# Kernel tuning notes

Measured on AMD Instinct MI355X. Metric: run time of the kernel, lower is better.

Reference implementation:

```python
import jax, jax.numpy as jnp
import numpy as np

B, L, HSIZE = 16, 512, 1024
H, D = 16, 64  # HHEAD = HSIZE/base, HBASE = 64

def setup_inputs() -> dict:
    key = jax.random.key(0)
    ks = jax.random.split(key, 10)
    inp = {
        'v': jax.random.normal(ks[0], (B, L, HSIZE), jnp.float32),
        'k': jax.random.normal(ks[1], (B, L, HSIZE), jnp.float32),
        'q': jax.random.normal(ks[2], (B, L, HSIZE), jnp.float32),
        'img_abs': jax.random.normal(ks[3], (B, L, HSIZE), jnp.float32),
        'Wv': jax.random.normal(ks[4], (HSIZE, HSIZE), jnp.float32) * 0.02,
        'Wk': jax.random.normal(ks[5], (HSIZE, HSIZE), jnp.float32) * 0.02,
        'Wq': jax.random.normal(ks[6], (HSIZE, HSIZE), jnp.float32) * 0.02,
        'Wm': jax.random.normal(ks[7], (HSIZE, HSIZE), jnp.float32) * 0.02,
        'abs_mask': jax.random.bernoulli(ks[8], 0.1, (B, 1, L, L)),
        'mask': jax.random.bernoulli(ks[9], 0.1, (B, 1, L, L)),
    }
    return inp

def reference(v, k, q, img_abs, Wv, Wk, Wq, Wm, abs_mask, mask):
    nb = q.shape[0]
    # Linear (no bias) then split heads: [B, L, HSIZE] -> [B, H, L, D]
    def heads(x):
        return x.reshape(nb, -1, H, D).transpose(0, 2, 1, 3)
    vh = heads(v @ Wv.T)
    kh = heads(k @ Wk.T)
    qh = heads(q @ Wq.T)
    ph = heads(img_abs)
    scale = 1.0 / jnp.sqrt(jnp.asarray(D, qh.dtype))
    # modulate: attention of q over positional features, residual-added to q
    s1 = jnp.einsum('bhqd,bhpd->bhqp', qh, ph) * scale
    s1 = jnp.where(abs_mask, jnp.asarray(-1e9, s1.dtype), s1)
    qh = qh + jnp.einsum('bhqp,bhpd->bhqd', jax.nn.softmax(s1, axis=-1), ph)
    # main attention (dropout = identity in eval mode)
    s2 = jnp.einsum('bhqd,bhkd->bhqk', qh, kh) * scale
    s2 = jnp.where(mask, jnp.asarray(-1e9, s2.dtype), s2)
    atted = jnp.einsum('bhqk,bhkd->bhqd', jax.nn.softmax(s2, axis=-1), vh)
    atted = atted.transpose(0, 2, 1, 3).reshape(nb, -1, H * D)
    return atted @ Wm.T
```

## Files before the change

kernel.cpp:

```cpp
#include <hip/hip_runtime.h>

typedef unsigned short u16;
typedef unsigned int u32;
typedef unsigned long long u64;
typedef __attribute__((ext_vector_type(8))) short short8;
typedef __attribute__((ext_vector_type(4))) float f32x4;

#define NB 16
#define SL 512
#define HS 1024
#define NHEAD 16
#define HD 64

typedef const __attribute__((address_space(1))) u32* gas_t;
typedef __attribute__((address_space(3))) u32* las_t;

__device__ __forceinline__ void gld16(const u16* g, u16* l) {
  __builtin_amdgcn_global_load_lds((gas_t)g, (las_t)l, 16, 0, 0);
}

__device__ __forceinline__ u16 f2bf(float f) {
  union { float f; unsigned u; } c; c.f = f;
  unsigned r = c.u + 0x7FFFu + ((c.u >> 16) & 1u);
  return (u16)(r >> 16);
}
__device__ __forceinline__ float bf2f(u16 u) {
  union { float f; unsigned u; } c; c.u = ((unsigned)u) << 16;
  return c.f;
}

__global__ __launch_bounds__(256) void cvt_bf16(const float* __restrict__ in,
                                                u16* __restrict__ out, long n) {
  long i = ((long)blockIdx.x * 256 + threadIdx.x) * 4;
  if (i >= n) return;
  float4 f = *(const float4*)(in + i);
  uint2 u;
  u.x = (unsigned)f2bf(f.x) | ((unsigned)f2bf(f.y) << 16);
  u.y = (unsigned)f2bf(f.z) | ((unsigned)f2bf(f.w) << 16);
  *(uint2*)(out + i) = u;
}

__global__ __launch_bounds__(256) void cvt_w4(const float* __restrict__ a,
                                              const float* __restrict__ b,
                                              const float* __restrict__ c,
                                              const float* __restrict__ d,
                                              u16* __restrict__ o, long n) {
  const float* in = (blockIdx.y == 0) ? a : (blockIdx.y == 1) ? b
                     : (blockIdx.y == 2) ? c : d;
  u16* out = o + (long)blockIdx.y * n;
  long i = ((long)blockIdx.x * 256 + threadIdx.x) * 4;
  if (i >= n) return;
  float4 f = *(const float4*)(in + i);
  uint2 u;
  u.x = (unsigned)f2bf(f.x) | ((unsigned)f2bf(f.y) << 16);
  u.y = (unsigned)f2bf(f.z) | ((unsigned)f2bf(f.w) << 16);
  *(uint2*)(out + i) = u;
}

__global__ __launch_bounds__(256) void pack_mask(const int* __restrict__ m0,
                                                 const int* __restrict__ m1,
                                                 u64* __restrict__ o0,
                                                 u64* __restrict__ o1, long n) {
  long i = (long)blockIdx.x * 256 + threadIdx.x;
  const int* m = blockIdx.y ? m1 : m0;
  u64* o = blockIdx.y ? o1 : o0;
  u64 bits = __ballot(m[i] != 0);
  if ((threadIdx.x & 63) == 0) o[i >> 6] = bits;
}

template<bool CF32>
__global__ __launch_bounds__(256) void gemm_bt(const u16* __restrict__ A,
                                               const u16* __restrict__ W,
                                               void* __restrict__ C,
                                               int M, int N, int K) {
  __shared__ u16 As[128 * 64];
  __shared__ u16 Bs[128 * 64];
  const int tid = threadIdx.x;
  const int wave = tid >> 6, lane = tid & 63;
  const int quad = lane >> 4, l16 = lane & 15;
  const int l7 = l16 & 7;
  const int row0 = blockIdx.x * 128, col0 = blockIdx.y * 128;
  const int wm = (wave >> 1) * 64, wn = (wave & 1) * 64;
  const int lrow = lane >> 3;
  const int scb = (lane & 7) ^ lrow;

  f32x4 acc[4][4];
#pragma unroll
  for (int mt = 0; mt < 4; ++mt)
#pragma unroll
    for (int nt = 0; nt < 4; ++nt) acc[mt][nt] = (f32x4){0.f, 0.f, 0.f, 0.f};

  const u16* Ab = A + (long)row0 * K;
  const u16* Wb = W + (long)col0 * K;

  for (int k0 = 0; k0 < K; k0 += 64) {
    __syncthreads();
#pragma unroll
    for (int it = 0; it < 4; ++it) {
      int seg = wave * 4 + it;
      int r = seg * 8 + lrow;
      gld16(Ab + (long)r * K + k0 + scb * 8, As + seg * 512);
      gld16(Wb + (long)r * K + k0 + scb * 8, Bs + seg * 512);
    }
    __syncthreads();
#pragma unroll
    for (int kt = 0; kt < 2; ++kt) {
      short8 af[4], bw[4];
#pragma unroll
      for (int mt = 0; mt < 4; ++mt)
        af[mt] = *(const short8*)(As + (wm + mt * 16 + l16) * 64 +
                                  (((kt * 4 + quad) ^ l7) * 8));
#pragma unroll
      for (int nt = 0; nt < 4; ++nt)
        bw[nt] = *(const short8*)(Bs + (wn + nt * 16 + l16) * 64 +
                                  (((kt * 4 + quad) ^ l7) * 8));
#pragma unroll
      for (int mt = 0; mt < 4; ++mt)
#pragma unroll
        for (int nt = 0; nt < 4; ++nt)
          acc[mt][nt] = __builtin_amdgcn_mfma_f32_16x16x32_bf16(
              af[mt], bw[nt], acc[mt][nt], 0, 0, 0);
    }
  }
#pragma unroll
  for (int mt = 0; mt < 4; ++mt)
#pragma unroll
    for (int nt = 0; nt < 4; ++nt)
#pragma unroll
      for (int i = 0; i < 4; ++i) {
        long r = row0 + wm + mt * 16 + quad * 4 + i;
        long c = col0 + wn + nt * 16 + l16;
        float v = acc[mt][nt][i];
        if constexpr (CF32)
          ((float*)C)[r * N + c] = v;
        else
          ((u16*)C)[r * N + c] = f2bf(v);
      }
}

__global__ __launch_bounds__(256) void attn(const u16* __restrict__ Qp,
                                            const u16* __restrict__ Kp,
                                            const u16* __restrict__ Vp,
                                            const u32* __restrict__ Bits,
                                            u16* __restrict__ Op,
                                            int residual) {
  __shared__ u16 Qs[64][72];
  __shared__ u16 Ks[64][72];
  __shared__ u16 Vs[64][72];
  __shared__ u16 Ps[64][72];
  const int tid = threadIdx.x;
  const int wave = tid >> 6, lane = tid & 63;
  const int quad = lane >> 4, l16 = lane & 15;
  const int qt = blockIdx.x, h = blockIdx.y, b = blockIdx.z;
  const int q0 = qt * 64;
  const long bs = (long)SL * HS;
  const u16* Qb = Qp + (long)b * bs + h * HD;
  const u16* Kb = Kp + (long)b * bs + h * HD;
  const u16* Vb = Vp + (long)b * bs + h * HD;
  const u32* Mb = Bits + (long)b * SL * 16;

  const int sr = tid >> 2, sds = (tid & 3) * 16;
  {
    const uint4* s = (const uint4*)(Qb + (long)(q0 + sr) * HS + sds);
    *(uint4*)&Qs[sr][sds] = s[0];
    *(uint4*)&Qs[sr][sds + 8] = s[1];
  }

  float l_i[4] = {0.f, 0.f, 0.f, 0.f};
  f32x4 o[4];
#pragma unroll
  for (int nt = 0; nt < 4; ++nt) o[nt] = (f32x4){0.f, 0.f, 0.f, 0.f};

  const int vxor = ((sds >> 4) & 3) << 4;
  const int vcol = sr ^ vxor;

  for (int t = 0; t < 8; ++t) {
    const int k0 = t * 64;
    __syncthreads();
    {
      const uint4* sk = (const uint4*)(Kb + (long)(k0 + sr) * HS + sds);
      *(uint4*)&Ks[sr][sds] = sk[0];
      *(uint4*)&Ks[sr][sds + 8] = sk[1];
      uint4 v0 = *(const uint4*)(Vb + (long)(k0 + sr) * HS + sds);
      uint4 v1 = *(const uint4*)(Vb + (long)(k0 + sr) * HS + sds + 8);
      union { uint4 q[2]; u16 e[16]; } tv;
      tv.q[0] = v0; tv.q[1] = v1;
#pragma unroll
      for (int j = 0; j < 16; ++j) Vs[sds + j][vcol] = tv.e[j];
    }
    __syncthreads();
    f32x4 s[4];
#pragma unroll
    for (int nt = 0; nt < 4; ++nt) s[nt] = (f32x4){0.f, 0.f, 0.f, 0.f};
#pragma unroll
    for (int kt = 0; kt < 2; ++kt) {
      short8 aq = *(const short8*)&Qs[wave * 16 + l16][kt * 32 + quad * 8];
#pragma unroll
      for (int nt = 0; nt < 4; ++nt) {
        short8 bk = *(const short8*)&Ks[nt * 16 + l16][kt * 32 + quad * 8];
        s[nt] = __builtin_amdgcn_mfma_f32_16x16x32_bf16(aq, bk, s[nt], 0, 0, 0);
      }
    }
#pragma unroll
    for (int i = 0; i < 4; ++i) {
      int gr = q0 + wave * 16 + quad * 4 + i;
      uint2 mw = *(const uint2*)&Mb[(long)gr * 16 + t * 2];
#pragma unroll
      for (int nt = 0; nt < 4; ++nt) {
        u32 w = (nt & 2) ? mw.y : mw.x;
        int msk = (w >> ((nt & 1) * 16 + l16)) & 1;
        float p = msk ? 0.f : __expf(s[nt][i] * 0.125f);
        s[nt][i] = p;
        l_i[i] += p;
      }
    }
#pragma unroll
    for (int i = 0; i < 4; ++i) {
      int prow = wave * 16 + quad * 4 + i;
#pragma unroll
      for (int nt = 0; nt < 4; ++nt)
        Ps[prow][(nt * 16 + l16) ^ (quad << 3)] = f2bf(s[nt][i]);
    }
    __syncthreads();
#pragma unroll
    for (int kt = 0; kt < 2; ++kt) {
      short8 ap = *(const short8*)&Ps[wave * 16 + l16]
                                    [(kt * 32 + quad * 8) ^ ((l16 >> 2) << 3)];
#pragma unroll
      for (int nt = 0; nt < 4; ++nt) {
        short8 bv = *(const short8*)&Vs[nt * 16 + l16]
                                      [(kt * 32 + quad * 8) ^ ((nt & 3) << 4)];
        o[nt] = __builtin_amdgcn_mfma_f32_16x16x32_bf16(ap, bv, o[nt], 0, 0, 0);
      }
    }
  }
  u16* Ob = Op + (long)b * bs + h * HD;
#pragma unroll
  for (int i = 0; i < 4; ++i) {
    float rs = l_i[i];
#pragma unroll
    for (int off = 8; off >= 1; off >>= 1) rs += __shfl_xor(rs, off, 64);
    float inv = 1.f / rs;
    int r = q0 + wave * 16 + quad * 4 + i;
#pragma unroll
    for (int nt = 0; nt < 4; ++nt) {
      float val = o[nt][i] * inv;
      if (residual) val += bf2f(Qs[wave * 16 + quad * 4 + i][nt * 16 + l16]);
      Ob[(long)r * HS + nt * 16 + l16] = f2bf(val);
    }
  }
}

extern "C" void kernel_launch(void* const* d_in, const int* in_sizes, int n_in,
                              void* d_out, int out_size, void* d_ws,
                              size_t ws_size, hipStream_t stream) {
  const float* v   = (const float*)d_in[0];
  const float* k   = (const float*)d_in[1];
  const float* q   = (const float*)d_in[2];
  const float* img = (const float*)d_in[3];
  const float* Wv  = (const float*)d_in[4];
  const float* Wk  = (const float*)d_in[5];
  const float* Wq  = (const float*)d_in[6];
  const float* Wm  = (const float*)d_in[7];
  const int* absm  = (const int*)d_in[8];
  const int* mask  = (const int*)d_in[9];
  float* out = (float*)d_out;

  const long NTOK = (long)NB * SL * HS;
  const long NW   = (long)HS * HS;
  const long NM   = (long)NB * SL * SL;
  u16* ws  = (u16*)d_ws;
  u16* xb  = ws;
  u16* pb  = ws + 1 * NTOK;
  u16* vh  = ws + 2 * NTOK;
  u16* kh  = ws + 3 * NTOK;
  u16* qh  = ws + 4 * NTOK;
  u16* w4  = ws + 5 * NTOK;
  u64* bt0 = (u64*)(w4 + 4 * NW);
  u64* bt1 = bt0 + NM / 64;
  u16* qm  = xb;
  u16* att = qh;

  dim3 gg(NB * SL / 128, HS / 128);
  dim3 ga(SL / 64, NHEAD, NB);

  cvt_bf16<<<(unsigned)(NTOK / 1024), 256, 0, stream>>>(img, pb, NTOK);
  cvt_w4<<<dim3((unsigned)(NW / 1024), 4), 256, 0, stream>>>(Wv, Wk, Wq, Wm, w4, NW);
  pack_mask<<<dim3((unsigned)(NM / 256), 2), 256, 0, stream>>>(absm, mask, bt0, bt1, NM);

  cvt_bf16<<<(unsigned)(NTOK / 1024), 256, 0, stream>>>(v, xb, NTOK);
  gemm_bt<false><<<gg, 256, 0, stream>>>(xb, w4 + 0 * NW, vh, NB * SL, HS, HS);
  cvt_bf16<<<(unsigned)(NTOK / 1024), 256, 0, stream>>>(k, xb, NTOK);
  gemm_bt<false><<<gg, 256, 0, stream>>>(xb, w4 + 1 * NW, kh, NB * SL, HS, HS);
  cvt_bf16<<<(unsigned)(NTOK / 1024), 256, 0, stream>>>(q, xb, NTOK);
  gemm_bt<false><<<gg, 256, 0, stream>>>(xb, w4 + 2 * NW, qh, NB * SL, HS, HS);

  attn<<<ga, 256, 0, stream>>>(qh, pb, pb, (const u32*)bt0, qm, 1);
  attn<<<ga, 256, 0, stream>>>(qm, kh, vh, (const u32*)bt1, att, 0);

  gemm_bt<true><<<gg, 256, 0, stream>>>(att, w4 + 3 * NW, out, NB * SL, HS, HS);
}
```

Before: 418.2 us.

## Batch input conversions and QKV projections, shrink output GEMM tile, register Q in attention

Fuses the four fp32-to-bf16 conversions into one launch, staging converted v and k in the output buffer as scratch. The three projection GEMMs become a single grouped launch selected by block index. The output projection gets a smaller 64x128 tile kernel with a higher occupancy hint, giving more blocks. In attention, Q fragments are loaded straight into registers instead of shared memory, the residual is read from global, and the XOR swizzle on the P tile is removed. The P-swizzle removal may bring back LDS bank conflicts.

```diff
diff --git a/kernel.cpp b/kernel.cpp
--- a/kernel.cpp
+++ b/kernel.cpp
@@ -11,6 +11,8 @@
 #define HS 1024
 #define NHEAD 16
 #define HD 64
+#define NTOKC (16L * 512 * 1024)
+#define NWC   (1024L * 1024)
 
 typedef const __attribute__((address_space(1))) u32* gas_t;
 typedef __attribute__((address_space(3))) u32* las_t;
@@ -29,8 +31,16 @@
   return c.f;
 }
 
-__global__ __launch_bounds__(256) void cvt_bf16(const float* __restrict__ in,
-                                                u16* __restrict__ out, long n) {
+__global__ __launch_bounds__(256) void cvt4(const float* __restrict__ v,
+                                            const float* __restrict__ k,
+                                            const float* __restrict__ q,
+                                            const float* __restrict__ img,
+                                            u16* __restrict__ ovk,
+                                            u16* __restrict__ xq,
+                                            u16* __restrict__ pb, long n) {
+  int which = blockIdx.y;
+  const float* in = which == 0 ? v : which == 1 ? k : which == 2 ? q : img;
+  u16* out = which == 0 ? ovk : which == 1 ? ovk + n : which == 2 ? xq : pb;
   long i = ((long)blockIdx.x * 256 + threadIdx.x) * 4;
   if (i >= n) return;
   float4 f = *(const float4*)(in + i);
@@ -68,21 +78,26 @@
   if ((threadIdx.x & 63) == 0) o[i >> 6] = bits;
 }
 
-template<bool CF32>
-__global__ __launch_bounds__(256) void gemm_bt(const u16* __restrict__ A,
-                                               const u16* __restrict__ W,
-                                               void* __restrict__ C,
-                                               int M, int N, int K) {
+__global__ __launch_bounds__(256) void gemm_p3(const u16* __restrict__ Avk,
+                                               const u16* __restrict__ Aq,
+                                               const u16* __restrict__ W4,
+                                               u16* __restrict__ Cb) {
   __shared__ u16 As[128 * 64];
   __shared__ u16 Bs[128 * 64];
   const int tid = threadIdx.x;
   const int wave = tid >> 6, lane = tid & 63;
   const int quad = lane >> 4, l16 = lane & 15;
   const int l7 = l16 & 7;
-  const int row0 = blockIdx.x * 128, col0 = blockIdx.y * 128;
+  const int sel = blockIdx.x >> 6;
+  const int row0 = (blockIdx.x & 63) * 128, col0 = blockIdx.y * 128;
   const int wm = (wave >> 1) * 64, wn = (wave & 1) * 64;
   const int lrow = lane >> 3;
   const int scb = (lane & 7) ^ lrow;
+  const int K = HS, N = HS;
+
+  const u16* A = (sel == 2) ? Aq : Avk + (long)sel * NTOKC;
+  const u16* W = W4 + (long)sel * NWC;
+  u16* C = Cb + (long)sel * NTOKC;
 
   f32x4 acc[4][4];
 #pragma unroll
@@ -130,11 +145,75 @@
       for (int i = 0; i < 4; ++i) {
         long r = row0 + wm + mt * 16 + quad * 4 + i;
         long c = col0 + wn + nt * 16 + l16;
-        float v = acc[mt][nt][i];
-        if constexpr (CF32)
-          ((float*)C)[r * N + c] = v;
-        else
-          ((u16*)C)[r * N + c] = f2bf(v);
+        C[r * N + c] = f2bf(acc[mt][nt][i]);
+      }
+}
+
+__global__ __launch_bounds__(256, 4) void gemm_f(const u16* __restrict__ A,
+                                                 const u16* __restrict__ W,
+                                                 float* __restrict__ C) {
+  __shared__ u16 As[64 * 64];
+  __shared__ u16 Bs[128 * 64];
+  const int tid = threadIdx.x;
+  const int wave = tid >> 6, lane = tid & 63;
+  const int quad = lane >> 4, l16 = lane & 15;
+  const int l7 = l16 & 7;
+  const int row0 = blockIdx.x * 64, col0 = blockIdx.y * 128;
+  const int wm = (wave >> 1) * 32, wn = (wave & 1) * 64;
+  const int lrow = lane >> 3;
+  const int scb = (lane & 7) ^ lrow;
+  const int K = HS, N = HS;
+
+  f32x4 acc[2][4];
+#pragma unroll
+  for (int mt = 0; mt < 2; ++mt)
+#pragma unroll
+    for (int nt = 0; nt < 4; ++nt) acc[mt][nt] = (f32x4){0.f, 0.f, 0.f, 0.f};
+
+  const u16* Ab = A + (long)row0 * K;
+  const u16* Wb = W + (long)col0 * K;
+
+  for (int k0 = 0; k0 < K; k0 += 64) {
+    __syncthreads();
+#pragma unroll
+    for (int it = 0; it < 2; ++it) {
+      int seg = wave * 2 + it;
+      gld16(Ab + (long)(seg * 8 + lrow) * K + k0 + scb * 8, As + seg * 512);
+    }
+#pragma unroll
+    for (int it = 0; it < 4; ++it) {
+      int seg = wave * 4 + it;
+      gld16(Wb + (long)(seg * 8 + lrow) * K + k0 + scb * 8, Bs + seg * 512);
+    }
+    __syncthreads();
+#pragma unroll
+    for (int kt = 0; kt < 2; ++kt) {
+      short8 af[2], bw[4];
+#pragma unroll
+      for (int mt = 0; mt < 2; ++mt)
+        af[mt] = *(const short8*)(As + (wm + mt * 16 + l16) * 64 +
+                                  (((kt * 4 + quad) ^ l7) * 8));
+#pragma unroll
+      for (int nt = 0; nt < 4; ++nt)
+        bw[nt] = *(const short8*)(Bs + (wn + nt * 16 + l16) * 64 +
+                                  (((kt * 4 + quad) ^ l7) * 8));
+#pragma unroll
+      for (int mt = 0; mt < 2; ++mt)
+#pragma unroll
+        for (int nt = 0; nt < 4; ++nt)
+          acc[mt][nt] = __builtin_amdgcn_mfma_f32_16x16x32_bf16(
+              af[mt], bw[nt], acc[mt][nt], 0, 0, 0);
+    }
+  }
+#pragma unroll
+  for (int mt = 0; mt < 2; ++mt)
+#pragma unroll
+    for (int nt = 0; nt < 4; ++nt)
+#pragma unroll
+      for (int i = 0; i < 4; ++i) {
+        long r = row0 + wm + mt * 16 + quad * 4 + i;
+        long c = col0 + wn + nt * 16 + l16;
+        C[r * N + c] = acc[mt][nt][i];
       }
 }
 
@@ -144,7 +223,6 @@
                                             const u32* __restrict__ Bits,
                                             u16* __restrict__ Op,
                                             int residual) {
-  __shared__ u16 Qs[64][72];
   __shared__ u16 Ks[64][72];
   __shared__ u16 Vs[64][72];
   __shared__ u16 Ps[64][72];
@@ -159,11 +237,11 @@
   const u16* Vb = Vp + (long)b * bs + h * HD;
   const u32* Mb = Bits + (long)b * SL * 16;
 
-  const int sr = tid >> 2, sds = (tid & 3) * 16;
-  {
-    const uint4* s = (const uint4*)(Qb + (long)(q0 + sr) * HS + sds);
-    *(uint4*)&Qs[sr][sds] = s[0];
-    *(uint4*)&Qs[sr][sds + 8] = s[1];
+  short8 qf[2];
+#pragma unroll
+  for (int kt = 0; kt < 2; ++kt) {
+    int row = q0 + wave * 16 + l16;
+    qf[kt] = *(const short8*)(Qb + (long)row * HS + kt * 32 + quad * 8);
   }
 
   float l_i[4] = {0.f, 0.f, 0.f, 0.f};
@@ -171,8 +249,8 @@
 #pragma unroll
   for (int nt = 0; nt < 4; ++nt) o[nt] = (f32x4){0.f, 0.f, 0.f, 0.f};
 
-  const int vxor = ((sds >> 4) & 3) << 4;
-  const int vcol = sr ^ vxor;
+  const int sr = tid >> 2, sds = (tid & 3) * 16;
+  const int vcol = sr ^ (((sds >> 4) & 3) << 4);
 
   for (int t = 0; t < 8; ++t) {
     const int k0 = t * 64;
@@ -193,14 +271,12 @@
 #pragma unroll
     for (int nt = 0; nt < 4; ++nt) s[nt] = (f32x4){0.f, 0.f, 0.f, 0.f};
 #pragma unroll
-    for (int kt = 0; kt < 2; ++kt) {
-      short8 aq = *(const short8*)&Qs[wave * 16 + l16][kt * 32 + quad * 8];
+    for (int kt = 0; kt < 2; ++kt)
 #pragma unroll
       for (int nt = 0; nt < 4; ++nt) {
         short8 bk = *(const short8*)&Ks[nt * 16 + l16][kt * 32 + quad * 8];
-        s[nt] = __builtin_amdgcn_mfma_f32_16x16x32_bf16(aq, bk, s[nt], 0, 0, 0);
-      }
-    }
+        s[nt] = __builtin_amdgcn_mfma_f32_16x16x32_bf16(qf[kt], bk, s[nt], 0, 0, 0);
+      }
 #pragma unroll
     for (int i = 0; i < 4; ++i) {
       int gr = q0 + wave * 16 + quad * 4 + i;
@@ -210,22 +286,14 @@
         u32 w = (nt & 2) ? mw.y : mw.x;
         int msk = (w >> ((nt & 1) * 16 + l16)) & 1;
         float p = msk ? 0.f : __expf(s[nt][i] * 0.125f);
-        s[nt][i] = p;
         l_i[i] += p;
-      }
-    }
-#pragma unroll
-    for (int i = 0; i < 4; ++i) {
-      int prow = wave * 16 + quad * 4 + i;
-#pragma unroll
-      for (int nt = 0; nt < 4; ++nt)
-        Ps[prow][(nt * 16 + l16) ^ (quad << 3)] = f2bf(s[nt][i]);
+        Ps[wave * 16 + quad * 4 + i][nt * 16 + l16] = f2bf(p);
+      }
     }
     __syncthreads();
 #pragma unroll
     for (int kt = 0; kt < 2; ++kt) {
-      short8 ap = *(const short8*)&Ps[wave * 16 + l16]
-                                    [(kt * 32 + quad * 8) ^ ((l16 >> 2) << 3)];
+      short8 ap = *(const short8*)&Ps[wave * 16 + l16][kt * 32 + quad * 8];
 #pragma unroll
       for (int nt = 0; nt < 4; ++nt) {
         short8 bv = *(const short8*)&Vs[nt * 16 + l16]
@@ -245,7 +313,7 @@
 #pragma unroll
     for (int nt = 0; nt < 4; ++nt) {
       float val = o[nt][i] * inv;
-      if (residual) val += bf2f(Qs[wave * 16 + quad * 4 + i][nt * 16 + l16]);
+      if (residual) val += bf2f(Qb[(long)r * HS + nt * 16 + l16]);
       Ob[(long)r * HS + nt * 16 + l16] = f2bf(val);
     }
   }
@@ -266,11 +334,12 @@
   const int* mask  = (const int*)d_in[9];
   float* out = (float*)d_out;
 
-  const long NTOK = (long)NB * SL * HS;
-  const long NW   = (long)HS * HS;
+  const long NTOK = NTOKC;
+  const long NW   = NWC;
   const long NM   = (long)NB * SL * SL;
+  u16* ovk = (u16*)d_out;
   u16* ws  = (u16*)d_ws;
-  u16* xb  = ws;
+  u16* xq  = ws;
   u16* pb  = ws + 1 * NTOK;
   u16* vh  = ws + 2 * NTOK;
   u16* kh  = ws + 3 * NTOK;
@@ -278,25 +347,19 @@
   u16* w4  = ws + 5 * NTOK;
   u64* bt0 = (u64*)(w4 + 4 * NW);
   u64* bt1 = bt0 + NM / 64;
-  u16* qm  = xb;
+  u16* qm  = xq;
   u16* att = qh;
 
-  dim3 gg(NB * SL / 128, HS / 128);
-  dim3 ga(SL / 64, NHEAD, NB);
-
-  cvt_bf16<<<(unsigned)(NTOK / 1024), 256, 0, stream>>>(img, pb, NTOK);
+  cvt4<<<dim3((unsigned)(NTOK / 1024), 4), 256, 0, stream>>>(v, k, q, img,
+                                                             ovk, xq, pb, NTOK);
   cvt_w4<<<dim3((unsigned)(NW / 1024), 4), 256, 0, stream>>>(Wv, Wk, Wq, Wm, w4, NW);
   pack_mask<<<dim3((unsigned)(NM / 256), 2), 256, 0, stream>>>(absm, mask, bt0, bt1, NM);
 
-  cvt_bf16<<<(unsigned)(NTOK / 1024), 256, 0, stream>>>(v, xb, NTOK);
-  gemm_bt<false><<<gg, 256, 0, stream>>>(xb, w4 + 0 * NW, vh, NB * SL, HS, HS);
-  cvt_bf16<<<(unsigned)(NTOK / 1024), 256, 0, stream>>>(k, xb, NTOK);
-  gemm_bt<false><<<gg, 256, 0, stream>>>(xb, w4 + 1 * NW, kh, NB * SL, HS, HS);
-  cvt_bf16<<<(unsigned)(NTOK / 1024), 256, 0, stream>>>(q, xb, NTOK);
-  gemm_bt<false><<<gg, 256, 0, stream>>>(xb, w4 + 2 * NW, qh, NB * SL, HS, HS);
-
+  gemm_p3<<<dim3(192, 8), 256, 0, stream>>>(ovk, xq, w4, vh);
+
+  dim3 ga(SL / 64, NHEAD, NB);
   attn<<<ga, 256, 0, stream>>>(qh, pb, pb, (const u32*)bt0, qm, 1);
   attn<<<ga, 256, 0, stream>>>(qm, kh, vh, (const u32*)bt1, att, 0);
 
-  gemm_bt<true><<<gg, 256, 0, stream>>>(att, w4 + 3 * NW, out, NB * SL, HS, HS);
-}
+  gemm_f<<<dim3(NB * SL / 64, HS / 128), 256, 0, stream>>>(att, w4 + 3 * NW, out);
+}
```

Result: no change. 425.5 us (+1.8%).
